# Kernel tuning notes

Measured on AMD Instinct MI355X. Metric: run time of the kernel, lower is better.

The kernel has to match this reference:

```python
import jax, jax.numpy as jnp
import numpy as np

N_NODES = 100000
N_EDGES = 1600000
IN_C, HID_C, OUT_C = 128, 128, 64
BN_EPS = 1e-5


def _sage_conv(x, src, dst, w_self, w_neigh, b):
    # mean aggregation over incoming edges (gather -> segment-sum -> scale)
    deg = jax.ops.segment_sum(jnp.ones((src.shape[0],), x.dtype), dst, num_segments=N_NODES)
    agg = jax.ops.segment_sum(x[src], dst, num_segments=N_NODES)
    agg = agg / jnp.maximum(deg, 1.0)[:, None]
    return x @ w_self + agg @ w_neigh + b


def _batch_norm(x, gamma, beta):
    mean = x.mean(axis=0)
    var = x.var(axis=0)
    return (x - mean) * jax.lax.rsqrt(var + BN_EPS) * gamma + beta


def setup_inputs() -> dict:
    key = jax.random.key(0)
    ks = jax.random.split(key, 16)
    x = jax.random.normal(ks[0], (N_NODES, IN_C), dtype=jnp.float32)
    edge_index = jax.random.randint(ks[1], (2, N_EDGES), 0, N_NODES, dtype=jnp.int64)
    s = 0.05
    return {
        "x": x,
        "edge_index": edge_index,
        "w0_self": jax.random.normal(ks[2], (IN_C, HID_C), jnp.float32) * s,
        "w0_neigh": jax.random.normal(ks[3], (IN_C, HID_C), jnp.float32) * s,
        "b0": jnp.zeros((HID_C,), jnp.float32),
        "g0": jnp.ones((HID_C,), jnp.float32),
        "be0": jnp.zeros((HID_C,), jnp.float32),
        "w1_self": jax.random.normal(ks[4], (HID_C, HID_C), jnp.float32) * s,
        "w1_neigh": jax.random.normal(ks[5], (HID_C, HID_C), jnp.float32) * s,
        "b1": jnp.zeros((HID_C,), jnp.float32),
        "g1": jnp.ones((HID_C,), jnp.float32),
        "be1": jnp.zeros((HID_C,), jnp.float32),
        "w2_self": jax.random.normal(ks[6], (HID_C, OUT_C), jnp.float32) * s,
        "w2_neigh": jax.random.normal(ks[7], (HID_C, OUT_C), jnp.float32) * s,
        "b2": jnp.zeros((OUT_C,), jnp.float32),
    }


def reference(x, edge_index, w0_self, w0_neigh, b0, g0, be0,
              w1_self, w1_neigh, b1, g1, be1, w2_self, w2_neigh, b2):
    src, dst = edge_index[0], edge_index[1]
    # layer 0: conv -> BN -> ReLU (dropout is identity in eval)
    h = _sage_conv(x, src, dst, w0_self, w0_neigh, b0)
    h = jax.nn.relu(_batch_norm(h, g0, be0))
    # layer 1
    h = _sage_conv(h, src, dst, w1_self, w1_neigh, b1)
    h = jax.nn.relu(_batch_norm(h, g1, be1))
    # final conv + log_softmax
    h = _sage_conv(h, src, dst, w2_self, w2_neigh, b2)
    return jax.nn.log_softmax(h, axis=-1)
```

## Files before the change

kernel.cpp:

```cpp
#include <hip/hip_runtime.h>

typedef unsigned int uint;
typedef __attribute__((ext_vector_type(8))) short short8;
typedef __attribute__((ext_vector_type(4))) float f32x4;

#define N_NODES 100000
#define N_EDGES 1600000
#define NB_SCAN 391
#define CONVG_N 1563

__device__ __forceinline__ float bflo(uint v) { return __uint_as_float(v << 16); }
__device__ __forceinline__ float bfhi(uint v) { return __uint_as_float(v & 0xffff0000u); }
__device__ __forceinline__ uint packbf2(float a, float b) {
    uint ua = __float_as_uint(a), ub = __float_as_uint(b);
    ua += 0x7fffu + ((ua >> 16) & 1u);
    ub += 0x7fffu + ((ub >> 16) & 1u);
    return (ua >> 16) | (ub & 0xffff0000u);
}

__global__ void deg_rank_kernel(const int* __restrict__ dst,
                                int* __restrict__ deg, int* __restrict__ rank) {
    int e = blockIdx.x * blockDim.x + threadIdx.x;
    if (e < N_EDGES) rank[e] = atomicAdd(&deg[dst[e]], 1);
}

__global__ void scan_blocksum(const int* __restrict__ deg, int* __restrict__ blk) {
    __shared__ int s[256];
    int i = blockIdx.x * 256 + threadIdx.x;
    s[threadIdx.x] = (i < N_NODES) ? deg[i] : 0;
    __syncthreads();
    for (int off = 128; off > 0; off >>= 1) {
        if (threadIdx.x < off) s[threadIdx.x] += s[threadIdx.x + off];
        __syncthreads();
    }
    if (threadIdx.x == 0) blk[blockIdx.x] = s[0];
}

__global__ void scan_blockoff(int* __restrict__ blk, int* __restrict__ row_ptr_last) {
    __shared__ int s[512];
    int t = threadIdx.x;
    int v = (t < NB_SCAN) ? blk[t] : 0;
    s[t] = v;
    __syncthreads();
    for (int off = 1; off < 512; off <<= 1) {
        int xv = (t >= off) ? s[t - off] : 0;
        __syncthreads();
        s[t] += xv;
        __syncthreads();
    }
    if (t < NB_SCAN) blk[t] = s[t] - v;
    if (t == NB_SCAN - 1) *row_ptr_last = s[t];
}

__global__ void scan_final(const int* __restrict__ deg, const int* __restrict__ blk,
                           int* __restrict__ row_ptr) {
    __shared__ int s[256];
    int i = blockIdx.x * 256 + threadIdx.x;
    int v = (i < N_NODES) ? deg[i] : 0;
    s[threadIdx.x] = v;
    __syncthreads();
    for (int off = 1; off < 256; off <<= 1) {
        int xv = (threadIdx.x >= off) ? s[threadIdx.x - off] : 0;
        __syncthreads();
        s[threadIdx.x] += xv;
        __syncthreads();
    }
    if (i < N_NODES) row_ptr[i] = blk[blockIdx.x] + s[threadIdx.x] - v;
}

__global__ void fill_csr2(const int* __restrict__ src, const int* __restrict__ dst,
                          const int* __restrict__ row_ptr, const int* __restrict__ rank,
                          int* __restrict__ colx) {
    int e = blockIdx.x * blockDim.x + threadIdx.x;
    if (e < N_EDGES) colx[row_ptr[dst[e]] + rank[e]] = src[e];
}

__global__ void invdeg_kernel(const int* __restrict__ deg, float* __restrict__ invd) {
    int i = blockIdx.x * blockDim.x + threadIdx.x;
    if (i < N_NODES) invd[i] = 1.0f / fmaxf((float)deg[i], 1.0f);
}

__global__ void transform_bf16(const float* __restrict__ H,
                               const float* __restrict__ scale, const float* __restrict__ shift,
                               uint* __restrict__ out2) {
    int i = blockIdx.x * blockDim.x + threadIdx.x;
    if (i >= N_NODES * 32) return;
    int row = i >> 5, q = i & 31;
    float4 v = *(const float4*)(H + (size_t)row * 128 + q * 4);
    if (scale) {
        int c = q * 4;
        v.x = fmaxf(v.x * scale[c]     + shift[c],     0.f);
        v.y = fmaxf(v.y * scale[c + 1] + shift[c + 1], 0.f);
        v.z = fmaxf(v.z * scale[c + 2] + shift[c + 2], 0.f);
        v.w = fmaxf(v.w * scale[c + 3] + shift[c + 3], 0.f);
    }
    uint2 o;
    o.x = packbf2(v.x, v.y);
    o.y = packbf2(v.z, v.w);
    *(uint2*)(out2 + (size_t)row * 64 + q * 2) = o;
}

__global__ void aggregate_bf16(const uint* __restrict__ H2,
                               const int* __restrict__ row_ptr, const int* __restrict__ colx,
                               const float* __restrict__ invd, uint* __restrict__ agg2) {
    int lane = threadIdx.x & 63;
    int node = blockIdx.x * 4 + (threadIdx.x >> 6);
    if (node >= N_NODES) return;
    int beg = row_ptr[node], end = row_ptr[node + 1];
    float a0 = 0.f, a1 = 0.f;
    int j = beg;
    for (; j + 8 <= end; j += 8) {
        int s0 = colx[j],     s1 = colx[j + 1], s2 = colx[j + 2], s3 = colx[j + 3];
        int s4 = colx[j + 4], s5 = colx[j + 5], s6 = colx[j + 6], s7 = colx[j + 7];
        uint v0 = H2[(size_t)s0 * 64 + lane];
        uint v1 = H2[(size_t)s1 * 64 + lane];
        uint v2 = H2[(size_t)s2 * 64 + lane];
        uint v3 = H2[(size_t)s3 * 64 + lane];
        uint v4 = H2[(size_t)s4 * 64 + lane];
        uint v5 = H2[(size_t)s5 * 64 + lane];
        uint v6 = H2[(size_t)s6 * 64 + lane];
        uint v7 = H2[(size_t)s7 * 64 + lane];
        a0 += (bflo(v0) + bflo(v1)) + (bflo(v2) + bflo(v3))
            + (bflo(v4) + bflo(v5)) + (bflo(v6) + bflo(v7));
        a1 += (bfhi(v0) + bfhi(v1)) + (bfhi(v2) + bfhi(v3))
            + (bfhi(v4) + bfhi(v5)) + (bfhi(v6) + bfhi(v7));
    }
    for (; j + 4 <= end; j += 4) {
        int s0 = colx[j], s1 = colx[j + 1], s2 = colx[j + 2], s3 = colx[j + 3];
        uint v0 = H2[(size_t)s0 * 64 + lane];
        uint v1 = H2[(size_t)s1 * 64 + lane];
        uint v2 = H2[(size_t)s2 * 64 + lane];
        uint v3 = H2[(size_t)s3 * 64 + lane];
        a0 += (bflo(v0) + bflo(v1)) + (bflo(v2) + bflo(v3));
        a1 += (bfhi(v0) + bfhi(v1)) + (bfhi(v2) + bfhi(v3));
    }
    for (; j < end; ++j) {
        uint v = H2[(size_t)colx[j] * 64 + lane];
        a0 += bflo(v);
        a1 += bfhi(v);
    }
    float id = invd[node];
    agg2[(size_t)node * 64 + lane] = packbf2(a0 * id, a1 * id);
}

template <int OUTC>
__global__ void pack_weights(const float* __restrict__ Wself, const float* __restrict__ Wneigh,
                             uint* __restrict__ Wb) {
    constexpr int NT = OUTC / 16;
    int i = blockIdx.x * 256 + threadIdx.x;
    if (i >= 8 * NT * 64 * 4) return;
    int u = i & 3;
    int l = (i >> 2) & 63;
    int t = i >> 8;
    int c = t % NT, s = t / NT;
    int k = s * 32 + (l >> 4) * 8 + u * 2;
    int col = c * 16 + (l & 15);
    const float* W0 = (k < 128) ? (Wself + (size_t)k * OUTC)
                                : (Wneigh + (size_t)(k - 128) * OUTC);
    const float* W1 = (k + 1 < 128) ? (Wself + (size_t)(k + 1) * OUTC)
                                    : (Wneigh + (size_t)(k + 1 - 128) * OUTC);
    Wb[i] = packbf2(W0[col], W1[col]);
}

template <int OUTC, bool STATS>
__global__ __launch_bounds__(256) void conv_mfma(
    const uint* __restrict__ Aself2, const uint* __restrict__ Agg2,
    const uint* __restrict__ Wb, const float* __restrict__ bias,
    float* __restrict__ Out, float* __restrict__ Ppart) {
    constexpr int NT = OUTC / 16;
    __shared__ float red[4][2 * OUTC];
    const int lane = threadIdx.x & 63;
    const int wv   = threadIdx.x >> 6;
    const int row0 = blockIdx.x * 64 + wv * 16;
    const int arow = row0 + (lane & 15);
    const bool aok = arow < N_NODES;
    const int kq   = lane >> 4;

    f32x4 acc[NT];
#pragma unroll
    for (int c = 0; c < NT; ++c) acc[c] = (f32x4){0.f, 0.f, 0.f, 0.f};

    union U { uint4 u; short8 s; };

#pragma unroll
    for (int s = 0; s < 8; ++s) {
        const uint* Asrc = (s < 4) ? Aself2 : Agg2;
        U a;
        a.u = make_uint4(0u, 0u, 0u, 0u);
        if (aok) a.u = *(const uint4*)(Asrc + (size_t)arow * 64 + (s & 3) * 16 + kq * 4);
#pragma unroll
        for (int c = 0; c < NT; ++c) {
            U b;
            b.u = *(const uint4*)(Wb + ((size_t)(s * NT + c) * 64 + lane) * 4);
            acc[c] = __builtin_amdgcn_mfma_f32_16x16x32_bf16(a.s, b.s, acc[c], 0, 0, 0);
        }
    }

    const int colbase = lane & 15;
#pragma unroll
    for (int c = 0; c < NT; ++c) {
        const int col = c * 16 + colbase;
        const float bv = bias[col];
        float sc = 0.f, qc = 0.f;
#pragma unroll
        for (int r = 0; r < 4; ++r) {
            int orow = row0 + kq * 4 + r;
            if (orow < N_NODES) {
                float v = acc[c][r] + bv;
                Out[(size_t)orow * OUTC + col] = v;
                if (STATS) { sc += v; qc += v * v; }
            }
        }
        if (STATS) {
            sc += __shfl_xor(sc, 16); sc += __shfl_xor(sc, 32);
            qc += __shfl_xor(qc, 16); qc += __shfl_xor(qc, 32);
            if (kq == 0) {
                red[wv][col]        = sc;
                red[wv][OUTC + col] = qc;
            }
        }
    }
    if (STATS) {
        __syncthreads();
        int t = threadIdx.x;
        if (t < 2 * OUTC) {
            float p = red[0][t] + red[1][t] + red[2][t] + red[3][t];
            Ppart[(size_t)blockIdx.x * (2 * OUTC) + t] = p;
        }
    }
}

template <int OUTC>
__global__ void bn_reduce(const float* __restrict__ Ppart, float* __restrict__ stats) {
    int t = threadIdx.x;
    float s = 0.f;
    for (int r = blockIdx.x; r < CONVG_N; r += gridDim.x)
        s += Ppart[(size_t)r * (2 * OUTC) + t];
    atomicAdd(&stats[t], s);
}

__global__ void bn_finalize(const float* __restrict__ stats,
                            const float* __restrict__ g, const float* __restrict__ be,
                            float* __restrict__ scale, float* __restrict__ shift) {
    int c = threadIdx.x;
    float mean = stats[c] * (1.0f / N_NODES);
    float var  = stats[128 + c] * (1.0f / N_NODES) - mean * mean;
    float inv  = rsqrtf(var + 1e-5f);
    float sc   = g[c] * inv;
    scale[c] = sc;
    shift[c] = be[c] - mean * sc;
}

__global__ void logsoftmax_k(float* __restrict__ out) {
    int lane = threadIdx.x & 63;
    int row = blockIdx.x * 4 + (threadIdx.x >> 6);
    if (row >= N_NODES) return;
    size_t base = (size_t)row * 64;
    float v = out[base + lane];
    float m = v;
#pragma unroll
    for (int o = 32; o > 0; o >>= 1) m = fmaxf(m, __shfl_xor(m, o));
    float e = expf(v - m);
    float ssum = e;
#pragma unroll
    for (int o = 32; o > 0; o >>= 1) ssum += __shfl_xor(ssum, o);
    out[base + lane] = v - m - logf(ssum);
}


extern "C" void kernel_launch(void* const* d_in, const int* in_sizes, int n_in,
                              void* d_out, int out_size, void* d_ws, size_t ws_size,
                              hipStream_t stream) {
    const float* x   = (const float*)d_in[0];
    const int*   ei  = (const int*)d_in[1];
    const float* w0s = (const float*)d_in[2];
    const float* w0n = (const float*)d_in[3];
    const float* b0  = (const float*)d_in[4];
    const float* g0  = (const float*)d_in[5];
    const float* be0 = (const float*)d_in[6];
    const float* w1s = (const float*)d_in[7];
    const float* w1n = (const float*)d_in[8];
    const float* b1  = (const float*)d_in[9];
    const float* g1  = (const float*)d_in[10];
    const float* be1 = (const float*)d_in[11];
    const float* w2s = (const float*)d_in[12];
    const float* w2n = (const float*)d_in[13];
    const float* b2  = (const float*)d_in[14];
    float* out = (float*)d_out;

    const int* src = ei;
    const int* dst = ei + N_EDGES;

    char* w = (char*)d_ws;
    size_t off = 0;
    auto alloc = [&](size_t bytes) {
        void* p = w + off;
        off += (bytes + 255) & ~(size_t)255;
        return p;
    };
    int*   deg     = (int*)alloc(N_NODES * 4);
    int*   row_ptr = (int*)alloc((N_NODES + 1) * 4);
    int*   blk     = (int*)alloc(512 * 4);
    int*   colx    = (int*)alloc((size_t)N_EDGES * 4);
    float* invd    = (float*)alloc(N_NODES * 4);
    float* stats   = (float*)alloc(256 * 4);
    float* scale0  = (float*)alloc(128 * 4);
    float* shift0  = (float*)alloc(128 * 4);
    float* scale1  = (float*)alloc(128 * 4);
    float* shift1  = (float*)alloc(128 * 4);
    uint*  wb0     = (uint*)alloc(16384 * 4);
    uint*  wb1     = (uint*)alloc(16384 * 4);
    uint*  wb2     = (uint*)alloc(8192 * 4);
    float* ppart   = (float*)alloc((size_t)CONVG_N * 256 * 4);
    uint*  ht2     = (uint*)alloc((size_t)N_NODES * 64 * 4);
    uint*  agg2    = (uint*)alloc((size_t)N_NODES * 64 * 4);
    float* h       = (float*)alloc((size_t)N_NODES * 128 * 4);
    int*   rank    = (int*)h;

    const int EB    = (N_EDGES + 255) / 256;
    const int NBk   = NB_SCAN;
    const int CONVG = CONVG_N;
    const int AGGG  = (N_NODES + 3) / 4;
    const int TFG   = (N_NODES * 32 + 255) / 256;

    hipMemsetAsync(deg, 0, N_NODES * 4, stream);
    deg_rank_kernel<<<EB, 256, 0, stream>>>(dst, deg, rank);
    scan_blocksum<<<NBk, 256, 0, stream>>>(deg, blk);
    scan_blockoff<<<1, 512, 0, stream>>>(blk, row_ptr + N_NODES);
    scan_final<<<NBk, 256, 0, stream>>>(deg, blk, row_ptr);
    fill_csr2<<<EB, 256, 0, stream>>>(src, dst, row_ptr, rank, colx);
    invdeg_kernel<<<NBk, 256, 0, stream>>>(deg, invd);
    pack_weights<128><<<64, 256, 0, stream>>>(w0s, w0n, wb0);
    pack_weights<128><<<64, 256, 0, stream>>>(w1s, w1n, wb1);
    pack_weights<64><<<32, 256, 0, stream>>>(w2s, w2n, wb2);

    transform_bf16<<<TFG, 256, 0, stream>>>(x, nullptr, nullptr, ht2);
    aggregate_bf16<<<AGGG, 256, 0, stream>>>(ht2, row_ptr, colx, invd, agg2);
    conv_mfma<128, true><<<CONVG, 256, 0, stream>>>(ht2, agg2, wb0, b0, h, ppart);
    hipMemsetAsync(stats, 0, 256 * 4, stream);
    bn_reduce<128><<<32, 256, 0, stream>>>(ppart, stats);
    bn_finalize<<<1, 128, 0, stream>>>(stats, g0, be0, scale0, shift0);

    transform_bf16<<<TFG, 256, 0, stream>>>(h, scale0, shift0, ht2);
    aggregate_bf16<<<AGGG, 256, 0, stream>>>(ht2, row_ptr, colx, invd, agg2);
    conv_mfma<128, true><<<CONVG, 256, 0, stream>>>(ht2, agg2, wb1, b1, h, ppart);
    hipMemsetAsync(stats, 0, 256 * 4, stream);
    bn_reduce<128><<<32, 256, 0, stream>>>(ppart, stats);
    bn_finalize<<<1, 128, 0, stream>>>(stats, g1, be1, scale1, shift1);

    transform_bf16<<<TFG, 256, 0, stream>>>(h, scale1, shift1, ht2);
    aggregate_bf16<<<AGGG, 256, 0, stream>>>(ht2, row_ptr, colx, invd, agg2);
    conv_mfma<64, false><<<CONVG, 256, 0, stream>>>(ht2, agg2, wb2, b2, out, nullptr);
    logsoftmax_k<<<AGGG, 256, 0, stream>>>(out);
}
```

Baseline: 484.2 us.

## Fuse BN+ReLU into aggregate and conv, emit bf16 hidden, fuse log_softmax

Drops the separate transform passes for layers 1 and 2. The BatchNorm scale/shift and ReLU are now applied on the fly to the gathered bf16 features in the aggregate kernel, and to the self-feature operand in the MFMA conv. The hidden-layer conv now writes bf16 instead of fp32, and it overwrites its own input buffer in place. The standalone log_softmax kernel is folded into the last conv epilogue using shuffles across 16-lane groups. This removes several full-array read/write passes and launches, at the cost of per-edge extra FMA/max work in the gather. BN statistics are still taken from fp32 values while normalization is applied to bf16-rounded values.

```diff
diff --git a/kernel.cpp b/kernel.cpp
--- a/kernel.cpp
+++ b/kernel.cpp
@@ -80,35 +80,41 @@
     if (i < N_NODES) invd[i] = 1.0f / fmaxf((float)deg[i], 1.0f);
 }
 
-__global__ void transform_bf16(const float* __restrict__ H,
-                               const float* __restrict__ scale, const float* __restrict__ shift,
-                               uint* __restrict__ out2) {
+__global__ void transform_f32(const float* __restrict__ H, uint* __restrict__ out2) {
     int i = blockIdx.x * blockDim.x + threadIdx.x;
     if (i >= N_NODES * 32) return;
     int row = i >> 5, q = i & 31;
     float4 v = *(const float4*)(H + (size_t)row * 128 + q * 4);
-    if (scale) {
-        int c = q * 4;
-        v.x = fmaxf(v.x * scale[c]     + shift[c],     0.f);
-        v.y = fmaxf(v.y * scale[c + 1] + shift[c + 1], 0.f);
-        v.z = fmaxf(v.z * scale[c + 2] + shift[c + 2], 0.f);
-        v.w = fmaxf(v.w * scale[c + 3] + shift[c + 3], 0.f);
-    }
     uint2 o;
     o.x = packbf2(v.x, v.y);
     o.y = packbf2(v.z, v.w);
     *(uint2*)(out2 + (size_t)row * 64 + q * 2) = o;
 }
 
+template <bool TF>
 __global__ void aggregate_bf16(const uint* __restrict__ H2,
+                               const float* __restrict__ scale, const float* __restrict__ shift,
                                const int* __restrict__ row_ptr, const int* __restrict__ colx,
                                const float* __restrict__ invd, uint* __restrict__ agg2) {
     int lane = threadIdx.x & 63;
     int node = blockIdx.x * 4 + (threadIdx.x >> 6);
     if (node >= N_NODES) return;
     int beg = row_ptr[node], end = row_ptr[node + 1];
+    float sc0 = 0.f, sc1 = 0.f, sh0 = 0.f, sh1 = 0.f;
+    if (TF) {
+        sc0 = scale[2 * lane];     sc1 = scale[2 * lane + 1];
+        sh0 = shift[2 * lane];     sh1 = shift[2 * lane + 1];
+    }
     float a0 = 0.f, a1 = 0.f;
     int j = beg;
+#define ACC1(v)                                                        \
+    if (TF) {                                                          \
+        a0 += fmaxf(bflo(v) * sc0 + sh0, 0.f);                         \
+        a1 += fmaxf(bfhi(v) * sc1 + sh1, 0.f);                         \
+    } else {                                                           \
+        a0 += bflo(v);                                                 \
+        a1 += bfhi(v);                                                 \
+    }
     for (; j + 8 <= end; j += 8) {
         int s0 = colx[j],     s1 = colx[j + 1], s2 = colx[j + 2], s3 = colx[j + 3];
         int s4 = colx[j + 4], s5 = colx[j + 5], s6 = colx[j + 6], s7 = colx[j + 7];
@@ -120,10 +126,7 @@
         uint v5 = H2[(size_t)s5 * 64 + lane];
         uint v6 = H2[(size_t)s6 * 64 + lane];
         uint v7 = H2[(size_t)s7 * 64 + lane];
-        a0 += (bflo(v0) + bflo(v1)) + (bflo(v2) + bflo(v3))
-            + (bflo(v4) + bflo(v5)) + (bflo(v6) + bflo(v7));
-        a1 += (bfhi(v0) + bfhi(v1)) + (bfhi(v2) + bfhi(v3))
-            + (bfhi(v4) + bfhi(v5)) + (bfhi(v6) + bfhi(v7));
+        ACC1(v0) ACC1(v1) ACC1(v2) ACC1(v3) ACC1(v4) ACC1(v5) ACC1(v6) ACC1(v7)
     }
     for (; j + 4 <= end; j += 4) {
         int s0 = colx[j], s1 = colx[j + 1], s2 = colx[j + 2], s3 = colx[j + 3];
@@ -131,14 +134,13 @@
         uint v1 = H2[(size_t)s1 * 64 + lane];
         uint v2 = H2[(size_t)s2 * 64 + lane];
         uint v3 = H2[(size_t)s3 * 64 + lane];
-        a0 += (bflo(v0) + bflo(v1)) + (bflo(v2) + bflo(v3));
-        a1 += (bfhi(v0) + bfhi(v1)) + (bfhi(v2) + bfhi(v3));
+        ACC1(v0) ACC1(v1) ACC1(v2) ACC1(v3)
     }
     for (; j < end; ++j) {
         uint v = H2[(size_t)colx[j] * 64 + lane];
-        a0 += bflo(v);
-        a1 += bfhi(v);
-    }
+        ACC1(v)
+    }
+#undef ACC1
     float id = invd[node];
     agg2[(size_t)node * 64 + lane] = packbf2(a0 * id, a1 * id);
 }
@@ -162,11 +164,12 @@
     Wb[i] = packbf2(W0[col], W1[col]);
 }
 
-template <int OUTC, bool STATS>
+template <int OUTC, bool STATS, bool BF16OUT, bool TF, bool LSM>
 __global__ __launch_bounds__(256) void conv_mfma(
     const uint* __restrict__ Aself2, const uint* __restrict__ Agg2,
     const uint* __restrict__ Wb, const float* __restrict__ bias,
-    float* __restrict__ Out, float* __restrict__ Ppart) {
+    const float* __restrict__ scale, const float* __restrict__ shift,
+    float* __restrict__ OutF, uint* __restrict__ OutB, float* __restrict__ Ppart) {
     constexpr int NT = OUTC / 16;
     __shared__ float red[4][2 * OUTC];
     const int lane = threadIdx.x & 63;
@@ -187,7 +190,24 @@
         const uint* Asrc = (s < 4) ? Aself2 : Agg2;
         U a;
         a.u = make_uint4(0u, 0u, 0u, 0u);
-        if (aok) a.u = *(const uint4*)(Asrc + (size_t)arow * 64 + (s & 3) * 16 + kq * 4);
+        if (aok) {
+            a.u = *(const uint4*)(Asrc + (size_t)arow * 64 + (s & 3) * 16 + kq * 4);
+            if (TF && s < 4) {
+                const int cb = (s & 3) * 32 + kq * 8;
+                float4 sa = *(const float4*)(scale + cb);
+                float4 sb = *(const float4*)(scale + cb + 4);
+                float4 ha = *(const float4*)(shift + cb);
+                float4 hb = *(const float4*)(shift + cb + 4);
+                a.u.x = packbf2(fmaxf(bflo(a.u.x) * sa.x + ha.x, 0.f),
+                                fmaxf(bfhi(a.u.x) * sa.y + ha.y, 0.f));
+                a.u.y = packbf2(fmaxf(bflo(a.u.y) * sa.z + ha.z, 0.f),
+                                fmaxf(bfhi(a.u.y) * sa.w + ha.w, 0.f));
+                a.u.z = packbf2(fmaxf(bflo(a.u.z) * sb.x + hb.x, 0.f),
+                                fmaxf(bfhi(a.u.z) * sb.y + hb.y, 0.f));
+                a.u.w = packbf2(fmaxf(bflo(a.u.w) * sb.z + hb.z, 0.f),
+                                fmaxf(bfhi(a.u.w) * sb.w + hb.w, 0.f));
+            }
+        }
 #pragma unroll
         for (int c = 0; c < NT; ++c) {
             U b;
@@ -197,6 +217,35 @@
     }
 
     const int colbase = lane & 15;
+
+    if (LSM) {
+        float vb[NT][4];
+#pragma unroll
+        for (int c = 0; c < NT; ++c) {
+            float bv = bias[c * 16 + colbase];
+#pragma unroll
+            for (int r = 0; r < 4; ++r) vb[c][r] = acc[c][r] + bv;
+        }
+#pragma unroll
+        for (int r = 0; r < 4; ++r) {
+            float m = fmaxf(fmaxf(vb[0][r], vb[1][r]), fmaxf(vb[2][r], vb[3][r]));
+#pragma unroll
+            for (int o = 8; o >= 1; o >>= 1) m = fmaxf(m, __shfl_xor(m, o));
+            float ssum = (expf(vb[0][r] - m) + expf(vb[1][r] - m))
+                       + (expf(vb[2][r] - m) + expf(vb[3][r] - m));
+#pragma unroll
+            for (int o = 8; o >= 1; o >>= 1) ssum += __shfl_xor(ssum, o);
+            float lg = m + logf(ssum);
+            int orow = row0 + kq * 4 + r;
+            if (orow < N_NODES) {
+#pragma unroll
+                for (int c = 0; c < NT; ++c)
+                    OutF[(size_t)orow * OUTC + c * 16 + colbase] = vb[c][r] - lg;
+            }
+        }
+        return;
+    }
+
 #pragma unroll
     for (int c = 0; c < NT; ++c) {
         const int col = c * 16 + colbase;
@@ -205,10 +254,19 @@
 #pragma unroll
         for (int r = 0; r < 4; ++r) {
             int orow = row0 + kq * 4 + r;
-            if (orow < N_NODES) {
-                float v = acc[c][r] + bv;
-                Out[(size_t)orow * OUTC + col] = v;
-                if (STATS) { sc += v; qc += v * v; }
+            float v = acc[c][r] + bv;
+            if (BF16OUT) {
+                float vo = __shfl_xor(v, 1);
+                if (orow < N_NODES) {
+                    if ((colbase & 1) == 0)
+                        OutB[(size_t)orow * (OUTC / 2) + (col >> 1)] = packbf2(v, vo);
+                    if (STATS) { sc += v; qc += v * v; }
+                }
+            } else {
+                if (orow < N_NODES) {
+                    OutF[(size_t)orow * OUTC + col] = v;
+                    if (STATS) { sc += v; qc += v * v; }
+                }
             }
         }
         if (STATS) {
@@ -249,22 +307,6 @@
     float sc   = g[c] * inv;
     scale[c] = sc;
     shift[c] = be[c] - mean * sc;
-}
-
-__global__ void logsoftmax_k(float* __restrict__ out) {
-    int lane = threadIdx.x & 63;
-    int row = blockIdx.x * 4 + (threadIdx.x >> 6);
-    if (row >= N_NODES) return;
-    size_t base = (size_t)row * 64;
-    float v = out[base + lane];
-    float m = v;
-#pragma unroll
-    for (int o = 32; o > 0; o >>= 1) m = fmaxf(m, __shfl_xor(m, o));
-    float e = expf(v - m);
-    float ssum = e;
-#pragma unroll
-    for (int o = 32; o > 0; o >>= 1) ssum += __shfl_xor(ssum, o);
-    out[base + lane] = v - m - logf(ssum);
 }
 
 
@@ -314,8 +356,8 @@
     float* ppart   = (float*)alloc((size_t)CONVG_N * 256 * 4);
     uint*  ht2     = (uint*)alloc((size_t)N_NODES * 64 * 4);
     uint*  agg2    = (uint*)alloc((size_t)N_NODES * 64 * 4);
-    float* h       = (float*)alloc((size_t)N_NODES * 128 * 4);
-    int*   rank    = (int*)h;
+    uint*  h2      = (uint*)alloc((size_t)N_NODES * 64 * 4);
+    int*   rank    = (int*)agg2;
 
     const int EB    = (N_EDGES + 255) / 256;
     const int NBk   = NB_SCAN;
@@ -334,22 +376,22 @@
     pack_weights<128><<<64, 256, 0, stream>>>(w1s, w1n, wb1);
     pack_weights<64><<<32, 256, 0, stream>>>(w2s, w2n, wb2);
 
-    transform_bf16<<<TFG, 256, 0, stream>>>(x, nullptr, nullptr, ht2);
-    aggregate_bf16<<<AGGG, 256, 0, stream>>>(ht2, row_ptr, colx, invd, agg2);
-    conv_mfma<128, true><<<CONVG, 256, 0, stream>>>(ht2, agg2, wb0, b0, h, ppart);
+    transform_f32<<<TFG, 256, 0, stream>>>(x, ht2);
+    aggregate_bf16<false><<<AGGG, 256, 0, stream>>>(ht2, nullptr, nullptr, row_ptr, colx, invd, agg2);
+    conv_mfma<128, true, true, false, false><<<CONVG, 256, 0, stream>>>(
+        ht2, agg2, wb0, b0, nullptr, nullptr, nullptr, h2, ppart);
     hipMemsetAsync(stats, 0, 256 * 4, stream);
     bn_reduce<128><<<32, 256, 0, stream>>>(ppart, stats);
     bn_finalize<<<1, 128, 0, stream>>>(stats, g0, be0, scale0, shift0);
 
-    transform_bf16<<<TFG, 256, 0, stream>>>(h, scale0, shift0, ht2);
-    aggregate_bf16<<<AGGG, 256, 0, stream>>>(ht2, row_ptr, colx, invd, agg2);
-    conv_mfma<128, true><<<CONVG, 256, 0, stream>>>(ht2, agg2, wb1, b1, h, ppart);
+    aggregate_bf16<true><<<AGGG, 256, 0, stream>>>(h2, scale0, shift0, row_ptr, colx, invd, agg2);
+    conv_mfma<128, true, true, true, false><<<CONVG, 256, 0, stream>>>(
+        h2, agg2, wb1, b1, scale0, shift0, nullptr, h2, ppart);
     hipMemsetAsync(stats, 0, 256 * 4, stream);
     bn_reduce<128><<<32, 256, 0, stream>>>(ppart, stats);
     bn_finalize<<<1, 128, 0, stream>>>(stats, g1, be1, scale1, shift1);
 
-    transform_bf16<<<TFG, 256, 0, stream>>>(h, scale1, shift1, ht2);
-    aggregate_bf16<<<AGGG, 256, 0, stream>>>(ht2, row_ptr, colx, invd, agg2);
-    conv_mfma<64, false><<<CONVG, 256, 0, stream>>>(ht2, agg2, wb2, b2, out, nullptr);
-    logsoftmax_k<<<AGGG, 256, 0, stream>>>(out);
-}
+    aggregate_bf16<true><<<AGGG, 256, 0, stream>>>(h2, scale1, shift1, row_ptr, colx, invd, agg2);
+    conv_mfma<64, false, false, true, true><<<CONVG, 256, 0, stream>>>(
+        h2, agg2, wb2, b2, scale1, shift1, out, nullptr, nullptr);
+}
```

After: 442.8 us. 1.09x faster.
